# Kernel optimization log

Hardware: AMD Instinct MI355X
Metric: run time of the kernel (lower is better)

Reference implementation:

```python
import jax, jax.numpy as jnp
import numpy as np

TOKEN_SIZE = 16
STRIDE = 8
EMBED_DIM = 512


def setup_inputs() -> dict:
    key = jax.random.key(0)
    k1, k2 = jax.random.split(key)
    B, S, D = 32, 4096, EMBED_DIM
    x = jax.random.normal(k1, (B, S, D), dtype=jnp.float32)
    fan_in = TOKEN_SIZE * D
    W = jax.random.normal(k2, (fan_in, D), dtype=jnp.float32) / np.sqrt(fan_in)
    b = jnp.zeros((D,), dtype=jnp.float32)
    gamma = jnp.ones((D,), dtype=jnp.float32)
    beta = jnp.zeros((D,), dtype=jnp.float32)
    return {"x": x, "W": W, "b": b, "gamma": gamma, "beta": beta}


def reference(x, W, b, gamma, beta):
    B, S, D = x.shape
    n_win = (S - TOKEN_SIZE) // STRIDE + 1
    # gather all sliding windows at once: [n_win, token_size] index matrix
    idx = jnp.arange(n_win)[:, None] * STRIDE + jnp.arange(TOKEN_SIZE)[None, :]
    win = x[:, idx, :]                       # [B, n_win, token_size, D]
    win = win.reshape(B, n_win, TOKEN_SIZE * D)  # flatten each window
    h = jnp.einsum('bnf,fd->bnd', win, W) + b    # batched GEMM
    h = jax.nn.gelu(h, approximate=False)        # torch GELU default = exact erf
    # LayerNorm over last dim (eps matches torch default 1e-5)
    mu = jnp.mean(h, axis=-1, keepdims=True)
    var = jnp.var(h, axis=-1, keepdims=True)
    h = (h - mu) * jax.lax.rsqrt(var + 1e-5)
    return h * gamma + beta                      # [B, n_win, D]
```

## Files before the change

kernel.cpp:

```cpp
#include <hip/hip_runtime.h>
#include <hip/hip_bf16.h>
#include <cstdint>

#define S_LEN 4096
#define D_DIM 512
#define NWIN  511
#define KDIM  8192
#define TR3   1032
#define ROWB  72

typedef __attribute__((ext_vector_type(8))) short short8;
typedef __attribute__((ext_vector_type(4))) short short4v;
typedef __attribute__((ext_vector_type(4))) float f32x4;

__device__ __forceinline__ unsigned short f2b(float f) {
    union { float f; unsigned int u; } v; v.f = f;
    unsigned int r = v.u + 0x7FFFu + ((v.u >> 16) & 1u);
    return (unsigned short)(r >> 16);
}

__global__ void wpack2_kernel(const float* __restrict__ W, short8* __restrict__ pk) {
    __shared__ float tile[64][68];
    const int b2 = blockIdx.x;
    const int s = b2 >> 3, w = b2 & 7;
    const int t = s >> 3, c0 = s & 7;
    const int tid = threadIdx.x;
    {
        int r = tid >> 2, c4 = (tid & 3) << 4;
        const float* src = W + (size_t)(t * 512 + c0 * 64 + r) * D_DIM + (w << 6) + c4;
#pragma unroll
        for (int j = 0; j < 4; ++j) {
            float4 v = *(const float4*)(src + 4 * j);
            tile[r][c4 + 4 * j + 0] = v.x;
            tile[r][c4 + 4 * j + 1] = v.y;
            tile[r][c4 + 4 * j + 2] = v.z;
            tile[r][c4 + 4 * j + 3] = v.w;
        }
    }
    __syncthreads();
    const int lane = tid & 63, f2 = tid >> 6;
    const int r15 = lane & 15, hi = lane >> 4;
#pragma unroll
    for (int ff = 0; ff < 2; ++ff) {
        int f = f2 * 2 + ff;
        int n = f >> 1, k32 = f & 1;
        int q2 = (c0 * 2 + k32) * 16 + t;
        short8 u;
#pragma unroll
        for (int e = 0; e < 8; ++e)
            u[e] = (short)f2b(tile[k32 * 32 + hi * 8 + e][n * 16 + r15]);
        pk[(size_t)q2 * 2048 + w * 256 + n * 64 + lane] = u;
    }
}

__global__ __launch_bounds__(512, 1)
void gemm3_kernel(const float* __restrict__ x,
                  const short8* __restrict__ pk,
                  const float* __restrict__ bias,
                  float* __restrict__ hbuf)
{
    __shared__ __align__(16) unsigned char lsA[2][TR3 * ROWB];

    const int bid = blockIdx.x;
    const int nc  = (bid & 7) >> 2;
    const int g   = ((bid >> 3) << 2) | (bid & 3);
    const int b   = g >> 2;
    const int win0 = (g & 3) << 7;
    const int tid = threadIdx.x;
    const int lane = tid & 63, wid = tid >> 6;
    const int wr = wid >> 2, wc = wid & 3;
    const int r15 = lane & 15, hi = lane >> 4;
    const int boff = ((nc * 4 + wc) << 8) + lane;
    const float* xb = x + (size_t)b * S_LEN * D_DIM;

    f32x4 acc[4][4] = {};
    short8 Bc[4], Bn[4];
    float4 ta[2][2];

#define CISSUE(J, Q)                                                           \
    {                                                                          \
        if ((J) < 8 || tid < 32) {                                             \
            const int c_ = tid + ((J) << 9);                                   \
            const int r_ = c_ >> 2, k4_ = c_ & 3;                              \
            int gr_ = (win0 << 3) + r_;                                        \
            if (gr_ > S_LEN - 1) gr_ = S_LEN - 1;                              \
            const float* s_ = xb + (size_t)gr_ * D_DIM + ((Q) << 5) + (k4_ << 3); \
            ta[(J) & 1][0] = *(const float4*)s_;                               \
            ta[(J) & 1][1] = *(const float4*)(s_ + 4);                         \
        }                                                                      \
    }

#define CWRITE(J, DST)                                                         \
    {                                                                          \
        if ((J) < 8 || tid < 32) {                                             \
            const int c_ = tid + ((J) << 9);                                   \
            const int r_ = c_ >> 2, k4_ = c_ & 3;                              \
            const int sw_ = (r_ >> 3) & 7;                                     \
            short4v lo_, hh_;                                                  \
            lo_[0] = (short)f2b(ta[(J) & 1][0].x);                             \
            lo_[1] = (short)f2b(ta[(J) & 1][0].y);                             \
            lo_[2] = (short)f2b(ta[(J) & 1][0].z);                             \
            lo_[3] = (short)f2b(ta[(J) & 1][0].w);                             \
            hh_[0] = (short)f2b(ta[(J) & 1][1].x);                             \
            hh_[1] = (short)f2b(ta[(J) & 1][1].y);                             \
            hh_[2] = (short)f2b(ta[(J) & 1][1].z);                             \
            hh_[3] = (short)f2b(ta[(J) & 1][1].w);                             \
            *(short4v*)&(DST)[r_ * ROWB + ((((k4_ << 1)    ) ^ sw_) << 3)] = lo_; \
            *(short4v*)&(DST)[r_ * ROWB + ((((k4_ << 1) | 1) ^ sw_) << 3)] = hh_; \
        }                                                                      \
    }

#define TSTEP(T, LA, BU, BL)                                                   \
    {                                                                          \
        const int q2n = (q16 + (T) + 1) & 255;                                 \
        _Pragma("unroll")                                                      \
        for (int n = 0; n < 4; ++n)                                            \
            BL[n] = pk[(size_t)q2n * 2048 + boff + n * 64];                    \
        __builtin_amdgcn_s_setprio(1);                                         \
        _Pragma("unroll")                                                      \
        for (int m = 0; m < 4; ++m) {                                          \
            const int wl_ = (wr << 6) + (m << 4) + r15;                        \
            const int r_ = (wl_ << 3) + (T);                                   \
            const int sw_ = (r_ >> 3) & 7;                                     \
            const unsigned char* rb_ = (LA) + r_ * ROWB;                       \
            short4v alo = *(const short4v*)&rb_[(((hi << 1)    ) ^ sw_) << 3]; \
            short4v ahi = *(const short4v*)&rb_[(((hi << 1) | 1) ^ sw_) << 3]; \
            short8 afr = __builtin_shufflevector(alo, ahi, 0, 1, 2, 3, 4, 5, 6, 7); \
            _Pragma("unroll")                                                  \
            for (int n = 0; n < 4; ++n)                                        \
                acc[m][n] = __builtin_amdgcn_mfma_f32_16x16x32_bf16(           \
                    afr, BU[n], acc[m][n], 0, 0, 0);                           \
        }                                                                      \
        __builtin_amdgcn_s_setprio(0);                                         \
    }

#pragma unroll
    for (int n = 0; n < 4; ++n)
        Bc[n] = pk[(size_t)boff + n * 64];
    CISSUE(0, 0) CISSUE(1, 0) CWRITE(0, lsA[0]) CISSUE(2, 0) CWRITE(1, lsA[0])
    CISSUE(3, 0) CWRITE(2, lsA[0]) CISSUE(4, 0) CWRITE(3, lsA[0])
    CISSUE(5, 0) CWRITE(4, lsA[0]) CISSUE(6, 0) CWRITE(5, lsA[0])
    CISSUE(7, 0) CWRITE(6, lsA[0]) CISSUE(8, 0) CWRITE(7, lsA[0])
    CWRITE(8, lsA[0])
    asm volatile("s_waitcnt lgkmcnt(0)" ::: "memory");
    __builtin_amdgcn_s_barrier();
    __builtin_amdgcn_sched_barrier(0);

    for (int sl = 0; sl < 16; ++sl) {
        const unsigned char* La = lsA[sl & 1];
        unsigned char* Ln = lsA[(sl + 1) & 1];
        const int q16 = sl << 4;
        const int qn = sl + 1;
        const int pf = (sl < 15);

        TSTEP(0, La, Bc, Bn)
        if (pf) { CISSUE(0, qn) CISSUE(1, qn) }
        TSTEP(1, La, Bn, Bc)
        if (pf) { CWRITE(0, Ln) CISSUE(2, qn) }
        TSTEP(2, La, Bc, Bn)
        if (pf) { CWRITE(1, Ln) CISSUE(3, qn) }
        TSTEP(3, La, Bn, Bc)
        if (pf) { CWRITE(2, Ln) CISSUE(4, qn) }
        TSTEP(4, La, Bc, Bn)
        if (pf) { CWRITE(3, Ln) CISSUE(5, qn) }
        TSTEP(5, La, Bn, Bc)
        if (pf) { CWRITE(4, Ln) CISSUE(6, qn) }
        TSTEP(6, La, Bc, Bn)
        if (pf) { CWRITE(5, Ln) CISSUE(7, qn) }
        TSTEP(7, La, Bn, Bc)
        if (pf) { CWRITE(6, Ln) CISSUE(8, qn) }
        TSTEP(8, La, Bc, Bn)
        if (pf) { CWRITE(7, Ln) }
        TSTEP(9, La, Bn, Bc)
        if (pf) { CWRITE(8, Ln) }
        TSTEP(10, La, Bc, Bn)
        TSTEP(11, La, Bn, Bc)
        TSTEP(12, La, Bc, Bn)
        TSTEP(13, La, Bn, Bc)
        TSTEP(14, La, Bc, Bn)
        TSTEP(15, La, Bn, Bc)

        asm volatile("s_waitcnt lgkmcnt(0)" ::: "memory");
        __builtin_amdgcn_s_barrier();
        __builtin_amdgcn_sched_barrier(0);
    }
#undef TSTEP
#undef CISSUE
#undef CWRITE

    const int dbase = ((nc * 4 + wc) << 6) + r15;
    float bias4[4];
#pragma unroll
    for (int n = 0; n < 4; ++n)
        bias4[n] = bias[dbase + (n << 4)];
    float* hb = hbuf + (size_t)b * NWIN * D_DIM;
#pragma unroll
    for (int m = 0; m < 4; ++m) {
#pragma unroll
        for (int r = 0; r < 4; ++r) {
            int win = win0 + (wr << 6) + (m << 4) + (hi << 2) + r;
            if (win < NWIN) {
                float* dst = hb + (size_t)win * D_DIM + dbase;
#pragma unroll
                for (int n = 0; n < 4; ++n) {
                    float h = acc[m][n][r] + bias4[n];
                    dst[n << 4] = 0.5f * h * (1.0f + erff(h * 0.70710678118654752f));
                }
            }
        }
    }
}

__global__ __launch_bounds__(256, 8)
void ln_kernel(const float* __restrict__ h, const float* __restrict__ gamma,
               const float* __restrict__ beta, float* __restrict__ out, int nrows)
{
    const int lane = threadIdx.x & 63;
    const int wv = blockIdx.x * 4 + (threadIdx.x >> 6);
    const int nw = gridDim.x * 4;
    float gm[8], bt[8];
#pragma unroll
    for (int j = 0; j < 8; ++j) {
        gm[j] = gamma[lane * 8 + j];
        bt[j] = beta[lane * 8 + j];
    }
    for (int row = wv; row < nrows; row += nw) {
        const float* src = h + (size_t)row * D_DIM + lane * 8;
        float4 v0 = *(const float4*)src;
        float4 v1 = *(const float4*)(src + 4);
        float s = v0.x + v0.y + v0.z + v0.w + v1.x + v1.y + v1.z + v1.w;
        float q = v0.x * v0.x + v0.y * v0.y + v0.z * v0.z + v0.w * v0.w +
                  v1.x * v1.x + v1.y * v1.y + v1.z * v1.z + v1.w * v1.w;
#pragma unroll
        for (int msk = 1; msk < 64; msk <<= 1) {
            s += __shfl_xor(s, msk, 64);
            q += __shfl_xor(q, msk, 64);
        }
        float mu  = s * (1.0f / 512.0f);
        float inv = rsqrtf(q * (1.0f / 512.0f) - mu * mu + 1e-5f);
        float o[8] = { v0.x, v0.y, v0.z, v0.w, v1.x, v1.y, v1.z, v1.w };
        float4 r0, r1;
        r0.x = (o[0] - mu) * inv * gm[0] + bt[0];
        r0.y = (o[1] - mu) * inv * gm[1] + bt[1];
        r0.z = (o[2] - mu) * inv * gm[2] + bt[2];
        r0.w = (o[3] - mu) * inv * gm[3] + bt[3];
        r1.x = (o[4] - mu) * inv * gm[4] + bt[4];
        r1.y = (o[5] - mu) * inv * gm[5] + bt[5];
        r1.z = (o[6] - mu) * inv * gm[6] + bt[6];
        r1.w = (o[7] - mu) * inv * gm[7] + bt[7];
        float* dst = out + (size_t)row * D_DIM + lane * 8;
        *(float4*)dst = r0;
        *(float4*)(dst + 4) = r1;
    }
}

__global__ void naive_kernel(const float* __restrict__ x, const float* __restrict__ W,
                             const float* __restrict__ bias, const float* __restrict__ gamma,
                             const float* __restrict__ beta, float* __restrict__ out) {
    __shared__ float hrow[D_DIM];
    __shared__ float red[2];
    const int b = blockIdx.x / NWIN, win = blockIdx.x % NWIN;
    const int d = threadIdx.x;
    float a = 0.f;
    for (int t = 0; t < 16; ++t) {
        const float* xr = x + ((size_t)b * S_LEN + 8 * win + t) * D_DIM;
        const float* wr = W + (size_t)t * D_DIM * D_DIM;
        for (int k = 0; k < D_DIM; ++k) a += xr[k] * wr[(size_t)k * D_DIM + d];
    }
    a += bias[d];
    a = 0.5f * a * (1.0f + erff(a * 0.70710678118654752f));
    hrow[d] = a;
    __syncthreads();
    if (d == 0) {
        float s = 0.f, q = 0.f;
        for (int k = 0; k < D_DIM; ++k) { s += hrow[k]; q += hrow[k] * hrow[k]; }
        float mu = s / D_DIM;
        red[0] = mu; red[1] = rsqrtf(q / D_DIM - mu * mu + 1e-5f);
    }
    __syncthreads();
    out[((size_t)b * NWIN + win) * D_DIM + d] = (a - red[0]) * red[1] * gamma[d] + beta[d];
}

extern "C" void kernel_launch(void* const* d_in, const int* in_sizes, int n_in,
                              void* d_out, int out_size, void* d_ws, size_t ws_size,
                              hipStream_t stream) {
    const float* x     = (const float*)d_in[0];
    const float* W     = (const float*)d_in[1];
    const float* bias  = (const float*)d_in[2];
    const float* gamma = (const float*)d_in[3];
    const float* beta  = (const float*)d_in[4];
    float* out = (float*)d_out;

    const size_t pk_bytes = (size_t)KDIM * D_DIM * sizeof(unsigned short);
    const size_t h_bytes  = (size_t)32 * NWIN * D_DIM * sizeof(float);

    if (ws_size >= pk_bytes + h_bytes) {
        short8* pk = (short8*)d_ws;
        float* hbuf = (float*)((char*)d_ws + pk_bytes);
        wpack2_kernel<<<1024, 256, 0, stream>>>(W, pk);
        gemm3_kernel<<<256, 512, 0, stream>>>(x, pk, bias, hbuf);
        ln_kernel<<<1024, 256, 0, stream>>>(hbuf, gamma, beta, out, 32 * NWIN);
    } else {
        naive_kernel<<<32 * NWIN, D_DIM, 0, stream>>>(x, W, bias, gamma, beta, out);
    }
}
```

Measured before the change: 194.2 us.

## Restructure GEMM main loop into two-step phases with barrier-fenced MFMA clusters

```diff
diff --git a/kernel.cpp b/kernel.cpp
--- a/kernel.cpp
+++ b/kernel.cpp
@@ -54,7 +54,7 @@
 }
 
 __global__ __launch_bounds__(512, 1)
-void gemm3_kernel(const float* __restrict__ x,
+void gemm4_kernel(const float* __restrict__ x,
                   const short8* __restrict__ pk,
                   const float* __restrict__ bias,
                   float* __restrict__ hbuf)
@@ -74,7 +74,7 @@
     const float* xb = x + (size_t)b * S_LEN * D_DIM;
 
     f32x4 acc[4][4] = {};
-    short8 Bc[4], Bn[4];
+    short8 Ba[8], Bb[8];
     float4 ta[2][2];
 
 #define CISSUE(J, Q)                                                           \
@@ -95,7 +95,7 @@
         if ((J) < 8 || tid < 32) {                                             \
             const int c_ = tid + ((J) << 9);                                   \
             const int r_ = c_ >> 2, k4_ = c_ & 3;                              \
-            const int sw_ = (r_ >> 3) & 7;                                     \
+            const int sw_ = ((r_ >> 3) & 7) ^ ((r_ >> 6) & 1);                 \
             short4v lo_, hh_;                                                  \
             lo_[0] = (short)f2b(ta[(J) & 1][0].x);                             \
             lo_[1] = (short)f2b(ta[(J) & 1][0].y);                             \
@@ -110,33 +110,47 @@
         }                                                                      \
     }
 
-#define TSTEP(T, LA, BU, BL)                                                   \
+#define PHASE(T0, BU, BL, EXTRA)                                               \
     {                                                                          \
-        const int q2n = (q16 + (T) + 1) & 255;                                 \
         _Pragma("unroll")                                                      \
-        for (int n = 0; n < 4; ++n)                                            \
-            BL[n] = pk[(size_t)q2n * 2048 + boff + n * 64];                    \
+        for (int j = 0; j < 8; ++j) {                                          \
+            const int q2n = (q16 + (T0) + 2 + (j >> 2)) & 255;                 \
+            BL[j] = pk[(size_t)q2n * 2048 + boff + (j & 3) * 64];              \
+        }                                                                      \
+        EXTRA                                                                  \
+        short8 af[8];                                                          \
+        _Pragma("unroll")                                                      \
+        for (int tt = 0; tt < 2; ++tt) {                                       \
+            _Pragma("unroll")                                                  \
+            for (int m = 0; m < 4; ++m) {                                      \
+                const int wl_ = (wr << 6) + (m << 4) + r15;                    \
+                const int r_ = (wl_ << 3) + (T0) + tt;                         \
+                const int sw_ = ((r_ >> 3) & 7) ^ ((r_ >> 6) & 1);             \
+                const unsigned char* rb_ = La + r_ * ROWB;                     \
+                short4v alo = *(const short4v*)&rb_[(((hi << 1)    ) ^ sw_) << 3]; \
+                short4v ahi = *(const short4v*)&rb_[(((hi << 1) | 1) ^ sw_) << 3]; \
+                af[tt * 4 + m] = __builtin_shufflevector(alo, ahi, 0, 1, 2, 3, 4, 5, 6, 7); \
+            }                                                                  \
+        }                                                                      \
+        __builtin_amdgcn_s_barrier();                                          \
+        asm volatile("s_waitcnt lgkmcnt(0)" ::: "memory");                     \
+        __builtin_amdgcn_sched_barrier(0);                                     \
         __builtin_amdgcn_s_setprio(1);                                         \
         _Pragma("unroll")                                                      \
-        for (int m = 0; m < 4; ++m) {                                          \
-            const int wl_ = (wr << 6) + (m << 4) + r15;                        \
-            const int r_ = (wl_ << 3) + (T);                                   \
-            const int sw_ = (r_ >> 3) & 7;                                     \
-            const unsigned char* rb_ = (LA) + r_ * ROWB;                       \
-            short4v alo = *(const short4v*)&rb_[(((hi << 1)    ) ^ sw_) << 3]; \
-            short4v ahi = *(const short4v*)&rb_[(((hi << 1) | 1) ^ sw_) << 3]; \
-            short8 afr = __builtin_shufflevector(alo, ahi, 0, 1, 2, 3, 4, 5, 6, 7); \
+        for (int tt = 0; tt < 2; ++tt)                                         \
             _Pragma("unroll")                                                  \
-            for (int n = 0; n < 4; ++n)                                        \
-                acc[m][n] = __builtin_amdgcn_mfma_f32_16x16x32_bf16(           \
-                    afr, BU[n], acc[m][n], 0, 0, 0);                           \
-        }                                                                      \
+            for (int m = 0; m < 4; ++m)                                        \
+                _Pragma("unroll")                                              \
+                for (int n = 0; n < 4; ++n)                                    \
+                    acc[m][n] = __builtin_amdgcn_mfma_f32_16x16x32_bf16(       \
+                        af[tt * 4 + m], BU[tt * 4 + n], acc[m][n], 0, 0, 0);   \
         __builtin_amdgcn_s_setprio(0);                                         \
-    }
-
-#pragma unroll
-    for (int n = 0; n < 4; ++n)
-        Bc[n] = pk[(size_t)boff + n * 64];
+        __builtin_amdgcn_s_barrier();                                          \
+    }
+
+#pragma unroll
+    for (int j = 0; j < 8; ++j)
+        Ba[j] = pk[(size_t)(j >> 2) * 2048 + boff + (j & 3) * 64];
     CISSUE(0, 0) CISSUE(1, 0) CWRITE(0, lsA[0]) CISSUE(2, 0) CWRITE(1, lsA[0])
     CISSUE(3, 0) CWRITE(2, lsA[0]) CISSUE(4, 0) CWRITE(3, lsA[0])
     CISSUE(5, 0) CWRITE(4, lsA[0]) CISSUE(6, 0) CWRITE(5, lsA[0])
@@ -153,38 +167,16 @@
         const int qn = sl + 1;
         const int pf = (sl < 15);
 
-        TSTEP(0, La, Bc, Bn)
-        if (pf) { CISSUE(0, qn) CISSUE(1, qn) }
-        TSTEP(1, La, Bn, Bc)
-        if (pf) { CWRITE(0, Ln) CISSUE(2, qn) }
-        TSTEP(2, La, Bc, Bn)
-        if (pf) { CWRITE(1, Ln) CISSUE(3, qn) }
-        TSTEP(3, La, Bn, Bc)
-        if (pf) { CWRITE(2, Ln) CISSUE(4, qn) }
-        TSTEP(4, La, Bc, Bn)
-        if (pf) { CWRITE(3, Ln) CISSUE(5, qn) }
-        TSTEP(5, La, Bn, Bc)
-        if (pf) { CWRITE(4, Ln) CISSUE(6, qn) }
-        TSTEP(6, La, Bc, Bn)
-        if (pf) { CWRITE(5, Ln) CISSUE(7, qn) }
-        TSTEP(7, La, Bn, Bc)
-        if (pf) { CWRITE(6, Ln) CISSUE(8, qn) }
-        TSTEP(8, La, Bc, Bn)
-        if (pf) { CWRITE(7, Ln) }
-        TSTEP(9, La, Bn, Bc)
-        if (pf) { CWRITE(8, Ln) }
-        TSTEP(10, La, Bc, Bn)
-        TSTEP(11, La, Bn, Bc)
-        TSTEP(12, La, Bc, Bn)
-        TSTEP(13, La, Bn, Bc)
-        TSTEP(14, La, Bc, Bn)
-        TSTEP(15, La, Bn, Bc)
-
-        asm volatile("s_waitcnt lgkmcnt(0)" ::: "memory");
-        __builtin_amdgcn_s_barrier();
-        __builtin_amdgcn_sched_barrier(0);
-    }
-#undef TSTEP
+        PHASE(0,  Ba, Bb, { if (pf) { CISSUE(0, qn) CISSUE(1, qn) } })
+        PHASE(2,  Bb, Ba, { if (pf) { CWRITE(0, Ln) CISSUE(2, qn) } })
+        PHASE(4,  Ba, Bb, { if (pf) { CWRITE(1, Ln) CISSUE(3, qn) } })
+        PHASE(6,  Bb, Ba, { if (pf) { CWRITE(2, Ln) CISSUE(4, qn) } })
+        PHASE(8,  Ba, Bb, { if (pf) { CWRITE(3, Ln) CISSUE(5, qn) } })
+        PHASE(10, Bb, Ba, { if (pf) { CWRITE(4, Ln) CISSUE(6, qn) } })
+        PHASE(12, Ba, Bb, { if (pf) { CWRITE(5, Ln) CISSUE(7, qn) CWRITE(6, Ln) } })
+        PHASE(14, Bb, Ba, { if (pf) { CISSUE(8, qn) CWRITE(7, Ln) CWRITE(8, Ln) } })
+    }
+#undef PHASE
 #undef CISSUE
 #undef CWRITE
 
@@ -298,7 +290,7 @@
         short8* pk = (short8*)d_ws;
         float* hbuf = (float*)((char*)d_ws + pk_bytes);
         wpack2_kernel<<<1024, 256, 0, stream>>>(W, pk);
-        gemm3_kernel<<<256, 512, 0, stream>>>(x, pk, bias, hbuf);
+        gemm4_kernel<<<256, 512, 0, stream>>>(x, pk, bias, hbuf);
         ln_kernel<<<1024, 256, 0, stream>>>(hbuf, gamma, beta, out, 32 * NWIN);
     } else {
         naive_kernel<<<32 * NWIN, D_DIM, 0, stream>>>(x, W, bias, gamma, beta, out);
```

New measurement: 373.1 us. 1.92x slower.
